# Optimization experiments

Measured on AMD Instinct MI355X. Metric: run time of the kernel, lower is better.

## Reference

```python
import jax, jax.numpy as jnp
import numpy as np

EMBED_DIM = 1024
NUM_HEADS = 16
HEAD_DIM = EMBED_DIM // NUM_HEADS
EPS = 1e-6


def setup_inputs() -> dict:
    key = jax.random.key(0)
    ks = jax.random.split(key, 10)
    B, S, D = 4, 2048, EMBED_DIM
    def xavier(k, shape):
        fan_in, fan_out = shape[1], shape[0]
        limit = float(np.sqrt(6.0 / (fan_in + fan_out)))
        return jax.random.uniform(k, shape, jnp.float32, -limit, limit)
    return {
        "x": jax.random.normal(ks[0], (B, S, D), jnp.float32),
        "ln_gamma": jnp.ones((D,), jnp.float32),
        "ln_beta": jnp.zeros((D,), jnp.float32),
        "Wq": xavier(ks[1], (D, D)), "bq": jnp.zeros((D,), jnp.float32),
        "Wk": xavier(ks[2], (D, D)), "bk": jnp.zeros((D,), jnp.float32),
        "Wv": xavier(ks[3], (D, D)), "bv": jnp.zeros((D,), jnp.float32),
        "Wo": xavier(ks[4], (D, D)), "bo": jnp.zeros((D,), jnp.float32),
    }


def reference(x, ln_gamma, ln_beta, Wq, bq, Wk, bk, Wv, bv, Wo, bo):
    B, S, D = x.shape
    # Pre-LayerNorm
    mu = jnp.mean(x, axis=-1, keepdims=True)
    var = jnp.mean((x - mu) ** 2, axis=-1, keepdims=True)
    xn = (x - mu) / jnp.sqrt(var + EPS) * ln_gamma + ln_beta
    # QKV projections (torch Linear: y = x @ W.T + b)
    def split_heads(t):  # [B,S,D] -> [B,H,S,hd]
        return t.reshape(B, S, NUM_HEADS, HEAD_DIM).transpose(0, 2, 1, 3)
    q = split_heads(xn @ Wq.T + bq)
    k = split_heads(xn @ Wk.T + bk)
    v = split_heads(xn @ Wv.T + bv)
    scale = 1.0 / jnp.sqrt(jnp.float32(HEAD_DIM))
    scores = jnp.einsum("bhqd,bhkd->bhqk", q, k) * scale
    probs = jax.nn.softmax(scores, axis=-1)  # dropout is identity (eval)
    ctx = jnp.einsum("bhqk,bhkd->bhqd", probs, v)
    ctx = ctx.transpose(0, 2, 1, 3).reshape(B, S, D)
    out = ctx @ Wo.T + bo  # proj dropout identity (eval)
    return out
```

## Files before the change

kernel.cpp:

```cpp
#include <hip/hip_runtime.h>
#include <hip/hip_bf16.h>
#include <stdint.h>

typedef __bf16 bf16x8 __attribute__((ext_vector_type(8)));
typedef float f32x4 __attribute__((ext_vector_type(4)));

#define LOG2E 1.44269504088896340736f

__device__ inline void gload_lds16(const void* g, void* l) {
  __builtin_amdgcn_global_load_lds((const __attribute__((address_space(1))) void*)g,
                                   (__attribute__((address_space(3))) void*)l, 16, 0, 0);
}

__device__ inline unsigned short bf16_bits(float f) {
  return __builtin_bit_cast(unsigned short, __float2bfloat16(f));
}

__device__ inline float fast_exp2(float x) {
  return __builtin_amdgcn_exp2f(x);
}

__device__ inline uint32_t cvtpk_bf16(float lo, float hi) {
  uint32_t d;
  asm("v_cvt_pk_bf16_f32 %0, %1, %2" : "=v"(d) : "v"(lo), "v"(hi));
  return d;
}
__device__ inline void plswap32(uint32_t& a, uint32_t& b) {
  asm("v_permlane32_swap_b32 %0, %1" : "+v"(a), "+v"(b));
}
__device__ inline void plswap16(uint32_t& a, uint32_t& b) {
  asm("v_permlane16_swap_b32 %0, %1" : "+v"(a), "+v"(b));
}

__global__ __launch_bounds__(256) void prep_kernel(
    const float* __restrict__ x, const float* __restrict__ gamma,
    const float* __restrict__ beta, __hip_bfloat16* __restrict__ xn,
    const float* __restrict__ Wq, const float* __restrict__ Wk,
    const float* __restrict__ Wv, const float* __restrict__ Wo,
    __hip_bfloat16* __restrict__ Wqk, __hip_bfloat16* __restrict__ Wvb,
    __hip_bfloat16* __restrict__ Wob)
{
  const int t = threadIdx.x;
  if (blockIdx.x < 8192) {
    const int row = blockIdx.x;
    const float4 v = reinterpret_cast<const float4*>(x + (size_t)row * 1024)[t];
    float s = v.x + v.y + v.z + v.w;
    float q = v.x*v.x + v.y*v.y + v.z*v.z + v.w*v.w;
    #pragma unroll
    for (int off = 32; off >= 1; off >>= 1) {
      s += __shfl_xor(s, off);
      q += __shfl_xor(q, off);
    }
    __shared__ float ls[4], lq[4];
    const int wave = t >> 6, lane = t & 63;
    if (lane == 0) { ls[wave] = s; lq[wave] = q; }
    __syncthreads();
    s = ls[0] + ls[1] + ls[2] + ls[3];
    q = lq[0] + lq[1] + lq[2] + lq[3];
    const float mean = s * (1.0f/1024.0f);
    const float var  = q * (1.0f/1024.0f) - mean*mean;
    const float rstd = rsqrtf(var + 1e-6f);
    const float4 gm = reinterpret_cast<const float4*>(gamma)[t];
    const float4 bt = reinterpret_cast<const float4*>(beta)[t];
    ushort4 o;
    o.x = bf16_bits((v.x - mean)*rstd*gm.x + bt.x);
    o.y = bf16_bits((v.y - mean)*rstd*gm.y + bt.y);
    o.z = bf16_bits((v.z - mean)*rstd*gm.z + bt.z);
    o.w = bf16_bits((v.w - mean)*rstd*gm.w + bt.w);
    reinterpret_cast<ushort4*>(xn + (size_t)row*1024)[t] = o;
  } else {
    const int cb = blockIdx.x - 8192;
    const int which = cb >> 10;
    const int i = (cb & 1023) * 256 + t;
    const float* src;
    __hip_bfloat16* dst;
    if (which == 0)      { src = Wq; dst = Wqk; }
    else if (which == 1) { src = Wk; dst = Wqk + 1024*1024; }
    else if (which == 2) { src = Wv; dst = Wvb; }
    else                 { src = Wo; dst = Wob; }
    const float4 v = reinterpret_cast<const float4*>(src)[i];
    ushort4 o;
    o.x = bf16_bits(v.x); o.y = bf16_bits(v.y);
    o.z = bf16_bits(v.z); o.w = bf16_bits(v.w);
    reinterpret_cast<ushort4*>(dst)[i] = o;
  }
}

__global__ __launch_bounds__(256) void qkv_gemm(
    const __hip_bfloat16* __restrict__ xn,
    const __hip_bfloat16* __restrict__ Wqk,
    const __hip_bfloat16* __restrict__ Wvb,
    const float* __restrict__ bq, const float* __restrict__ bk,
    const float* __restrict__ bv,
    __hip_bfloat16* __restrict__ Qb, __hip_bfloat16* __restrict__ Kb,
    __hip_bfloat16* __restrict__ Vt)
{
  constexpr int K = 1024;
  __shared__ __align__(16) __hip_bfloat16 Al[128*32];
  __shared__ __align__(16) __hip_bfloat16 Bl[128*32];
  const int t = threadIdx.x;
  const int wave = t >> 6, lane = t & 63;
  const int li = lane & 15, g = lane >> 4;
  const int wm = (wave >> 1) * 64, wn = (wave & 1) * 64;

  const int lin = blockIdx.x;
  const int wg  = (lin & 7) * 192 + (lin >> 3);
  const bool isV = wg >= 1024;
  int m0, n0;
  const __hip_bfloat16 *A, *B;
  if (!isV) {
    m0 = (wg >> 4) * 128; n0 = (wg & 15) * 128;
    A = xn; B = Wqk;
  } else {
    const int w2 = wg - 1024;
    m0 = (w2 & 7) * 128; n0 = (w2 >> 3) * 128;
    A = Wvb; B = xn;
  }
  const int srow = t >> 2, sch = (t & 3) * 8;

  const __hip_bfloat16* ga = A + (size_t)(m0 + srow) * K + sch;
  const __hip_bfloat16* gb = B + (size_t)(n0 + srow) * K + sch;

  f32x4 acc[4][4] = {};

  for (int kt = 0; kt < K; kt += 32) {
    gload_lds16(ga + kt,          Al + t*8);
    gload_lds16(ga + kt + 64*K,   Al + t*8 + 2048);
    gload_lds16(gb + kt,          Bl + t*8);
    gload_lds16(gb + kt + 64*K,   Bl + t*8 + 2048);
    __syncthreads();
    bf16x8 af[4], bfr[4];
    #pragma unroll
    for (int mi = 0; mi < 4; ++mi)
      af[mi] = *reinterpret_cast<const bf16x8*>(Al + (wm + mi*16 + li)*32 + g*8);
    #pragma unroll
    for (int ni = 0; ni < 4; ++ni)
      bfr[ni] = *reinterpret_cast<const bf16x8*>(Bl + (wn + ni*16 + li)*32 + g*8);
    #pragma unroll
    for (int mi = 0; mi < 4; ++mi)
      #pragma unroll
      for (int ni = 0; ni < 4; ++ni)
        acc[mi][ni] = __builtin_amdgcn_mfma_f32_16x16x32_bf16(af[mi], bfr[ni], acc[mi][ni], 0, 0, 0);
    __syncthreads();
  }

  #pragma unroll
  for (int mi = 0; mi < 4; ++mi) {
    #pragma unroll
    for (int ni = 0; ni < 4; ++ni) {
      #pragma unroll
      for (int r = 0; r < 4; ++r) {
        const int grow = m0 + wm + mi*16 + g*4 + r;
        const int gcol = n0 + wn + ni*16 + li;
        float v = acc[mi][ni][r];
        if (!isV) {
          const int b = grow >> 11, ss = grow & 2047;
          if (gcol < 1024) {
            v = (v + bq[gcol]) * (0.125f * LOG2E);
            const int h = gcol >> 6, d = gcol & 63;
            Qb[(((size_t)(b*16 + h))*2048 + ss)*64 + d] = __float2bfloat16(v);
          } else {
            const int c2 = gcol - 1024;
            v = v + bk[c2];
            const int h = c2 >> 6, d = c2 & 63;
            Kb[(((size_t)(b*16 + h))*2048 + ss)*64 + d] = __float2bfloat16(v);
          }
        } else {
          v += bv[grow];
          Vt[(size_t)grow*8192 + gcol] = __float2bfloat16(v);
        }
      }
    }
  }
}

__global__ __launch_bounds__(256) void out_gemm(
    const __hip_bfloat16* __restrict__ A,
    const __hip_bfloat16* __restrict__ B,
    const float* __restrict__ bias,
    float* __restrict__ C)
{
  constexpr int K = 1024;
  __shared__ __align__(16) __hip_bfloat16 Al[128*32];
  __shared__ __align__(16) __hip_bfloat16 Bl[128*32];
  const int t = threadIdx.x;
  const int wave = t >> 6, lane = t & 63;
  const int li = lane & 15, g = lane >> 4;
  const int wm = (wave >> 1) * 64, wn = (wave & 1) * 64;

  const int lin = blockIdx.y * gridDim.x + blockIdx.x;
  const int cpx = (gridDim.x * gridDim.y) >> 3;
  const int wg  = (lin & 7) * cpx + (lin >> 3);
  const int bx  = wg & (gridDim.x - 1);
  const int by  = wg >> __builtin_ctz(gridDim.x);
  const int m0 = by * 128, n0 = bx * 128;
  const int srow = t >> 2, sch = (t & 3) * 8;

  const __hip_bfloat16* ga = A + (size_t)(m0 + srow) * K + sch;
  const __hip_bfloat16* gb = B + (size_t)(n0 + srow) * K + sch;

  f32x4 acc[4][4] = {};

  for (int kt = 0; kt < K; kt += 32) {
    gload_lds16(ga + kt,          Al + t*8);
    gload_lds16(ga + kt + 64*K,   Al + t*8 + 2048);
    gload_lds16(gb + kt,          Bl + t*8);
    gload_lds16(gb + kt + 64*K,   Bl + t*8 + 2048);
    __syncthreads();
    bf16x8 af[4], bfr[4];
    #pragma unroll
    for (int mi = 0; mi < 4; ++mi)
      af[mi] = *reinterpret_cast<const bf16x8*>(Al + (wm + mi*16 + li)*32 + g*8);
    #pragma unroll
    for (int ni = 0; ni < 4; ++ni)
      bfr[ni] = *reinterpret_cast<const bf16x8*>(Bl + (wn + ni*16 + li)*32 + g*8);
    #pragma unroll
    for (int mi = 0; mi < 4; ++mi)
      #pragma unroll
      for (int ni = 0; ni < 4; ++ni)
        acc[mi][ni] = __builtin_amdgcn_mfma_f32_16x16x32_bf16(af[mi], bfr[ni], acc[mi][ni], 0, 0, 0);
    __syncthreads();
  }

  #pragma unroll
  for (int mi = 0; mi < 4; ++mi) {
    #pragma unroll
    for (int ni = 0; ni < 4; ++ni) {
      #pragma unroll
      for (int r = 0; r < 4; ++r) {
        const int grow = m0 + wm + mi*16 + g*4 + r;
        const int gcol = n0 + wn + ni*16 + li;
        C[(size_t)grow*1024 + gcol] = acc[mi][ni][r] + bias[gcol];
      }
    }
  }
}

__global__ __launch_bounds__(256, 4) void attn_kernel(
    const __hip_bfloat16* __restrict__ Q,
    const __hip_bfloat16* __restrict__ K,
    const __hip_bfloat16* __restrict__ Vt,
    __hip_bfloat16* __restrict__ ctx)
{
  const int t = threadIdx.x, wave = t >> 6, lane = t & 63;
  const int li = lane & 15, g = lane >> 4;

  const int lin = blockIdx.x;
  const int wg  = (lin & 7) * 128 + (lin >> 3);
  const int bh  = wg >> 4, qt = wg & 15;
  const int b = bh >> 4, h = bh & 15;
  const int qbase = qt * 128 + wave * 32;

  __shared__ __align__(16) __hip_bfloat16 Klds[2][4096];
  __shared__ __align__(16) __hip_bfloat16 Vlds[2][4096];

  const bf16x8* Qv0 = reinterpret_cast<const bf16x8*>(Q + ((size_t)bh*2048 + qbase + li)*64 + g*8);
  const bf16x8* Qv1 = reinterpret_cast<const bf16x8*>(Q + ((size_t)bh*2048 + qbase + 16 + li)*64 + g*8);
  const bf16x8 aQ00 = Qv0[0], aQ01 = Qv0[4];
  const bf16x8 aQ10 = Qv1[0], aQ11 = Qv1[4];

  f32x4 acc0[4] = {}, acc1[4] = {};
  float l0 = 0.f, l1 = 0.f;

  const __hip_bfloat16* Kbh = K + (size_t)bh*2048*64;
  const __hip_bfloat16* Vbh = Vt + (size_t)h*64*8192 + b*2048;

  const int l8 = lane >> 3;
  const int scb_e = ((((lane & 7) * 16) ^ (l8 << 4)) >> 1);
  const int row0 = wave * 8 + l8;

  const int krd0 = (li*128 + ((g*16)      ^ ((li & 7) << 4))) >> 1;
  const int krd1 = (li*128 + ((g*16 + 64) ^ ((li & 7) << 4))) >> 1;

  gload_lds16(Kbh + (size_t)row0*64 + scb_e,          &Klds[0][wave*512]);
  gload_lds16(Kbh + (size_t)(32+row0)*64 + scb_e,     &Klds[0][2048 + wave*512]);
  gload_lds16(Vbh + (size_t)row0*8192 + scb_e,        &Vlds[0][wave*512]);
  gload_lds16(Vbh + (size_t)(32+row0)*8192 + scb_e,   &Vlds[0][2048 + wave*512]);
  gload_lds16(Kbh + (size_t)(64+row0)*64 + scb_e,     &Klds[1][wave*512]);
  gload_lds16(Kbh + (size_t)(96+row0)*64 + scb_e,     &Klds[1][2048 + wave*512]);
  gload_lds16(Vbh + (size_t)row0*8192 + 64 + scb_e,   &Vlds[1][wave*512]);
  gload_lds16(Vbh + (size_t)(32+row0)*8192 + 64 + scb_e, &Vlds[1][2048 + wave*512]);
  asm volatile("s_waitcnt vmcnt(4)" ::: "memory");
  __builtin_amdgcn_sched_barrier(0);
  __builtin_amdgcn_s_barrier();

  const __hip_bfloat16* kSrc = Kbh + (size_t)(128 + row0)*64 + scb_e;
  const __hip_bfloat16* vSrc = Vbh + (size_t)row0*8192 + 128 + scb_e;

  for (int it = 0; it < 32; ++it) {
    const int cur = it & 1;
    const __hip_bfloat16* Kc = Klds[cur];
    const __hip_bfloat16* Vc = Vlds[cur];

    f32x4 s0[4] = {}, s1[4] = {};
    __builtin_amdgcn_s_setprio(1);
    #pragma unroll
    for (int nt = 0; nt < 4; ++nt) {
      const bf16x8 k0 = *reinterpret_cast<const bf16x8*>(&Kc[nt*1024 + krd0]);
      const bf16x8 k1 = *reinterpret_cast<const bf16x8*>(&Kc[nt*1024 + krd1]);
      s0[nt] = __builtin_amdgcn_mfma_f32_16x16x32_bf16(k0, aQ00, s0[nt], 0, 0, 0);
      s0[nt] = __builtin_amdgcn_mfma_f32_16x16x32_bf16(k1, aQ01, s0[nt], 0, 0, 0);
      s1[nt] = __builtin_amdgcn_mfma_f32_16x16x32_bf16(k0, aQ10, s1[nt], 0, 0, 0);
      s1[nt] = __builtin_amdgcn_mfma_f32_16x16x32_bf16(k1, aQ11, s1[nt], 0, 0, 0);
    }
    __builtin_amdgcn_s_setprio(0);

    float sm0 = 0.f, sm1 = 0.f;
    #pragma unroll
    for (int nt = 0; nt < 4; ++nt)
      #pragma unroll
      for (int r = 0; r < 4; ++r) {
        const float p0 = fast_exp2(s0[nt][r]); s0[nt][r] = p0; sm0 += p0;
        const float p1 = fast_exp2(s1[nt][r]); s1[nt][r] = p1; sm1 += p1;
      }
    l0 += sm0; l1 += sm1;

    union U8 { uint32_t w[4]; bf16x8 v; };
    bf16x8 aP00, aP01, aP10, aP11;
    {
      uint32_t c[4][2];
      #pragma unroll
      for (int nt = 0; nt < 4; ++nt) {
        c[nt][0] = cvtpk_bf16(s0[nt][0], s0[nt][1]);
        c[nt][1] = cvtpk_bf16(s0[nt][2], s0[nt][3]);
      }
      uint32_t x0 = c[0][0], y0 = c[1][0], x1 = c[0][1], y1 = c[1][1];
      plswap32(x0, y0); plswap32(x1, y1);
      plswap16(x0, y0); plswap16(x1, y1);
      U8 u0; u0.w[0] = x0; u0.w[1] = x1; u0.w[2] = y0; u0.w[3] = y1;
      aP00 = u0.v;
      uint32_t x2 = c[2][0], y2 = c[3][0], x3 = c[2][1], y3 = c[3][1];
      plswap32(x2, y2); plswap32(x3, y3);
      plswap16(x2, y2); plswap16(x3, y3);
      U8 u1; u1.w[0] = x2; u1.w[1] = x3; u1.w[2] = y2; u1.w[3] = y3;
      aP01 = u1.v;
    }
    {
      uint32_t c[4][2];
      #pragma unroll
      for (int nt = 0; nt < 4; ++nt) {
        c[nt][0] = cvtpk_bf16(s1[nt][0], s1[nt][1]);
        c[nt][1] = cvtpk_bf16(s1[nt][2], s1[nt][3]);
      }
      uint32_t x0 = c[0][0], y0 = c[1][0], x1 = c[0][1], y1 = c[1][1];
      plswap32(x0, y0); plswap32(x1, y1);
      plswap16(x0, y0); plswap16(x1, y1);
      U8 u0; u0.w[0] = x0; u0.w[1] = x1; u0.w[2] = y0; u0.w[3] = y1;
      aP10 = u0.v;
      uint32_t x2 = c[2][0], y2 = c[3][0], x3 = c[2][1], y3 = c[3][1];
      plswap32(x2, y2); plswap32(x3, y3);
      plswap16(x2, y2); plswap16(x3, y3);
      U8 u1; u1.w[0] = x2; u1.w[1] = x3; u1.w[2] = y2; u1.w[3] = y3;
      aP11 = u1.v;
    }

    __builtin_amdgcn_s_setprio(1);
    #pragma unroll
    for (int dt = 0; dt < 4; ++dt) {
      const bf16x8 v0 = *reinterpret_cast<const bf16x8*>(&Vc[dt*1024 + krd0]);
      const bf16x8 v1 = *reinterpret_cast<const bf16x8*>(&Vc[dt*1024 + krd1]);
      acc0[dt] = __builtin_amdgcn_mfma_f32_16x16x32_bf16(v0, aP00, acc0[dt], 0, 0, 0);
      acc0[dt] = __builtin_amdgcn_mfma_f32_16x16x32_bf16(v1, aP01, acc0[dt], 0, 0, 0);
      acc1[dt] = __builtin_amdgcn_mfma_f32_16x16x32_bf16(v0, aP10, acc1[dt], 0, 0, 0);
      acc1[dt] = __builtin_amdgcn_mfma_f32_16x16x32_bf16(v1, aP11, acc1[dt], 0, 0, 0);
    }
    __builtin_amdgcn_s_setprio(0);

    if (it < 31) {
      __builtin_amdgcn_s_barrier();
      if (it < 30) {
        gload_lds16(kSrc,           &Klds[cur][wave*512]);
        gload_lds16(kSrc + 32*64,   &Klds[cur][2048 + wave*512]);
        gload_lds16(vSrc,           &Vlds[cur][wave*512]);
        gload_lds16(vSrc + 32*8192, &Vlds[cur][2048 + wave*512]);
        kSrc += 64*64;
        vSrc += 64;
        asm volatile("s_waitcnt vmcnt(4)" ::: "memory");
      } else {
        asm volatile("s_waitcnt vmcnt(0)" ::: "memory");
      }
      __builtin_amdgcn_sched_barrier(0);
      __builtin_amdgcn_s_barrier();
    }
  }

  l0 += __shfl_xor(l0, 16); l0 += __shfl_xor(l0, 32);
  l1 += __shfl_xor(l1, 16); l1 += __shfl_xor(l1, 32);
  const float inv0 = 1.0f / l0;
  const float inv1 = 1.0f / l1;

  __hip_bfloat16* cp = ctx + ((size_t)(b*2048 + qbase))*1024 + h*64;
  #pragma unroll
  for (int dt = 0; dt < 4; ++dt) {
    ushort4 o0, o1;
    o0.x = bf16_bits(acc0[dt][0] * inv0);
    o0.y = bf16_bits(acc0[dt][1] * inv0);
    o0.z = bf16_bits(acc0[dt][2] * inv0);
    o0.w = bf16_bits(acc0[dt][3] * inv0);
    *reinterpret_cast<ushort4*>(&cp[(size_t)li*1024 + dt*16 + g*4]) = o0;
    o1.x = bf16_bits(acc1[dt][0] * inv1);
    o1.y = bf16_bits(acc1[dt][1] * inv1);
    o1.z = bf16_bits(acc1[dt][2] * inv1);
    o1.w = bf16_bits(acc1[dt][3] * inv1);
    *reinterpret_cast<ushort4*>(&cp[(size_t)(16 + li)*1024 + dt*16 + g*4]) = o1;
  }
}

extern "C" void kernel_launch(void* const* d_in, const int* in_sizes, int n_in,
                              void* d_out, int out_size, void* d_ws, size_t ws_size,
                              hipStream_t stream)
{
  const float* x  = (const float*)d_in[0];
  const float* g  = (const float*)d_in[1];
  const float* be = (const float*)d_in[2];
  const float* Wq = (const float*)d_in[3];
  const float* bq = (const float*)d_in[4];
  const float* Wk = (const float*)d_in[5];
  const float* bk = (const float*)d_in[6];
  const float* Wv = (const float*)d_in[7];
  const float* bv = (const float*)d_in[8];
  const float* Wo = (const float*)d_in[9];
  const float* bo = (const float*)d_in[10];
  float* out = (float*)d_out;

  char* ws = (char*)d_ws;
  __hip_bfloat16* xn  = (__hip_bfloat16*)(ws);
  __hip_bfloat16* Wqk = (__hip_bfloat16*)(ws + 16777216);
  __hip_bfloat16* Wvb = (__hip_bfloat16*)(ws + 20971520);
  __hip_bfloat16* Wob = (__hip_bfloat16*)(ws + 23068672);
  __hip_bfloat16* Qb  = (__hip_bfloat16*)(ws + 25165824);
  __hip_bfloat16* Kb  = (__hip_bfloat16*)(ws + 41943040);
  __hip_bfloat16* Vt  = (__hip_bfloat16*)(ws + 58720256);
  __hip_bfloat16* ctx = (__hip_bfloat16*)(ws + 75497472);

  prep_kernel<<<12288, 256, 0, stream>>>(x, g, be, xn, Wq, Wk, Wv, Wo, Wqk, Wvb, Wob);
  qkv_gemm<<<1536, 256, 0, stream>>>(xn, Wqk, Wvb, bq, bk, bv, Qb, Kb, Vt);
  attn_kernel<<<1024, 256, 0, stream>>>(Qb, Kb, Vt, ctx);
  out_gemm<<<dim3(8, 64), 256, 0, stream>>>(ctx, Wob, bo, out);
}
```

Baseline: 198.6 us.

## Split attention query tile across eight waves with 16 rows each

The attention block grows from 4 to 8 waves (512 threads), and each wave now handles 16 query rows instead of 32. K/V tile loads into LDS are spread over all 512 threads, so each thread issues half as many global-to-LDS loads per stage. The aim is more waves in flight and lower per-wave register pressure to hide MFMA and exp latency. The cost is that each K/V LDS fragment now feeds only one 16-row query tile per wave, which halves operand reuse from LDS reads, and the barriers now synchronise twice as many waves.

After: 203.4 us. +2.4%, slower.

```diff
diff --git a/kernel.cpp b/kernel.cpp
--- a/kernel.cpp
+++ b/kernel.cpp
@@ -236,7 +236,7 @@
   }
 }
 
-__global__ __launch_bounds__(256, 4) void attn_kernel(
+__global__ __launch_bounds__(512, 8) void attn_kernel(
     const __hip_bfloat16* __restrict__ Q,
     const __hip_bfloat16* __restrict__ K,
     const __hip_bfloat16* __restrict__ Vt,
@@ -249,38 +249,31 @@
   const int wg  = (lin & 7) * 128 + (lin >> 3);
   const int bh  = wg >> 4, qt = wg & 15;
   const int b = bh >> 4, h = bh & 15;
-  const int qbase = qt * 128 + wave * 32;
+  const int qbase = qt * 128 + wave * 16;
 
   __shared__ __align__(16) __hip_bfloat16 Klds[2][4096];
   __shared__ __align__(16) __hip_bfloat16 Vlds[2][4096];
 
-  const bf16x8* Qv0 = reinterpret_cast<const bf16x8*>(Q + ((size_t)bh*2048 + qbase + li)*64 + g*8);
-  const bf16x8* Qv1 = reinterpret_cast<const bf16x8*>(Q + ((size_t)bh*2048 + qbase + 16 + li)*64 + g*8);
-  const bf16x8 aQ00 = Qv0[0], aQ01 = Qv0[4];
-  const bf16x8 aQ10 = Qv1[0], aQ11 = Qv1[4];
-
-  f32x4 acc0[4] = {}, acc1[4] = {};
-  float l0 = 0.f, l1 = 0.f;
+  const bf16x8* Qv = reinterpret_cast<const bf16x8*>(Q + ((size_t)bh*2048 + qbase + li)*64 + g*8);
+  const bf16x8 aQ0 = Qv[0], aQ1 = Qv[4];
+
+  f32x4 acc[4] = {};
+  float l_par = 0.f;
 
   const __hip_bfloat16* Kbh = K + (size_t)bh*2048*64;
   const __hip_bfloat16* Vbh = Vt + (size_t)h*64*8192 + b*2048;
 
-  const int l8 = lane >> 3;
-  const int scb_e = ((((lane & 7) * 16) ^ (l8 << 4)) >> 1);
-  const int row0 = wave * 8 + l8;
+  const int row0 = t >> 3;
+  const int scb_e = ((((t & 7) * 16) ^ ((row0 & 7) << 4)) >> 1);
 
   const int krd0 = (li*128 + ((g*16)      ^ ((li & 7) << 4))) >> 1;
   const int krd1 = (li*128 + ((g*16 + 64) ^ ((li & 7) << 4))) >> 1;
 
-  gload_lds16(Kbh + (size_t)row0*64 + scb_e,          &Klds[0][wave*512]);
-  gload_lds16(Kbh + (size_t)(32+row0)*64 + scb_e,     &Klds[0][2048 + wave*512]);
-  gload_lds16(Vbh + (size_t)row0*8192 + scb_e,        &Vlds[0][wave*512]);
-  gload_lds16(Vbh + (size_t)(32+row0)*8192 + scb_e,   &Vlds[0][2048 + wave*512]);
-  gload_lds16(Kbh + (size_t)(64+row0)*64 + scb_e,     &Klds[1][wave*512]);
-  gload_lds16(Kbh + (size_t)(96+row0)*64 + scb_e,     &Klds[1][2048 + wave*512]);
-  gload_lds16(Vbh + (size_t)row0*8192 + 64 + scb_e,   &Vlds[1][wave*512]);
-  gload_lds16(Vbh + (size_t)(32+row0)*8192 + 64 + scb_e, &Vlds[1][2048 + wave*512]);
-  asm volatile("s_waitcnt vmcnt(4)" ::: "memory");
+  gload_lds16(Kbh + (size_t)row0*64 + scb_e,        &Klds[0][t*8]);
+  gload_lds16(Vbh + (size_t)row0*8192 + scb_e,      &Vlds[0][t*8]);
+  gload_lds16(Kbh + (size_t)(64+row0)*64 + scb_e,   &Klds[1][t*8]);
+  gload_lds16(Vbh + (size_t)row0*8192 + 64 + scb_e, &Vlds[1][t*8]);
+  asm volatile("s_waitcnt vmcnt(2)" ::: "memory");
   __builtin_amdgcn_sched_barrier(0);
   __builtin_amdgcn_s_barrier();
 
@@ -292,66 +285,45 @@
     const __hip_bfloat16* Kc = Klds[cur];
     const __hip_bfloat16* Vc = Vlds[cur];
 
-    f32x4 s0[4] = {}, s1[4] = {};
+    f32x4 s[4] = {};
     __builtin_amdgcn_s_setprio(1);
     #pragma unroll
     for (int nt = 0; nt < 4; ++nt) {
       const bf16x8 k0 = *reinterpret_cast<const bf16x8*>(&Kc[nt*1024 + krd0]);
       const bf16x8 k1 = *reinterpret_cast<const bf16x8*>(&Kc[nt*1024 + krd1]);
-      s0[nt] = __builtin_amdgcn_mfma_f32_16x16x32_bf16(k0, aQ00, s0[nt], 0, 0, 0);
-      s0[nt] = __builtin_amdgcn_mfma_f32_16x16x32_bf16(k1, aQ01, s0[nt], 0, 0, 0);
-      s1[nt] = __builtin_amdgcn_mfma_f32_16x16x32_bf16(k0, aQ10, s1[nt], 0, 0, 0);
-      s1[nt] = __builtin_amdgcn_mfma_f32_16x16x32_bf16(k1, aQ11, s1[nt], 0, 0, 0);
+      s[nt] = __builtin_amdgcn_mfma_f32_16x16x32_bf16(k0, aQ0, s[nt], 0, 0, 0);
+      s[nt] = __builtin_amdgcn_mfma_f32_16x16x32_bf16(k1, aQ1, s[nt], 0, 0, 0);
     }
     __builtin_amdgcn_s_setprio(0);
 
-    float sm0 = 0.f, sm1 = 0.f;
+    float sm = 0.f;
     #pragma unroll
     for (int nt = 0; nt < 4; ++nt)
       #pragma unroll
       for (int r = 0; r < 4; ++r) {
-        const float p0 = fast_exp2(s0[nt][r]); s0[nt][r] = p0; sm0 += p0;
-        const float p1 = fast_exp2(s1[nt][r]); s1[nt][r] = p1; sm1 += p1;
+        const float p = fast_exp2(s[nt][r]); s[nt][r] = p; sm += p;
       }
-    l0 += sm0; l1 += sm1;
+    l_par += sm;
 
     union U8 { uint32_t w[4]; bf16x8 v; };
-    bf16x8 aP00, aP01, aP10, aP11;
+    bf16x8 aP0, aP1;
     {
       uint32_t c[4][2];
       #pragma unroll
       for (int nt = 0; nt < 4; ++nt) {
-        c[nt][0] = cvtpk_bf16(s0[nt][0], s0[nt][1]);
-        c[nt][1] = cvtpk_bf16(s0[nt][2], s0[nt][3]);
+        c[nt][0] = cvtpk_bf16(s[nt][0], s[nt][1]);
+        c[nt][1] = cvtpk_bf16(s[nt][2], s[nt][3]);
       }
       uint32_t x0 = c[0][0], y0 = c[1][0], x1 = c[0][1], y1 = c[1][1];
       plswap32(x0, y0); plswap32(x1, y1);
       plswap16(x0, y0); plswap16(x1, y1);
       U8 u0; u0.w[0] = x0; u0.w[1] = x1; u0.w[2] = y0; u0.w[3] = y1;
-      aP00 = u0.v;
+      aP0 = u0.v;
       uint32_t x2 = c[2][0], y2 = c[3][0], x3 = c[2][1], y3 = c[3][1];
       plswap32(x2, y2); plswap32(x3, y3);
       plswap16(x2, y2); plswap16(x3, y3);
       U8 u1; u1.w[0] = x2; u1.w[1] = x3; u1.w[2] = y2; u1.w[3] = y3;
-      aP01 = u1.v;
-    }
-    {
-      uint32_t c[4][2];
-      #pragma unroll
-      for (int nt = 0; nt < 4; ++nt) {
-        c[nt][0] = cvtpk_bf16(s1[nt][0], s1[nt][1]);
-        c[nt][1] = cvtpk_bf16(s1[nt][2], s1[nt][3]);
-      }
-      uint32_t x0 = c[0][0], y0 = c[1][0], x1 = c[0][1], y1 = c[1][1];
-      plswap32(x0, y0); plswap32(x1, y1);
-      plswap16(x0, y0); plswap16(x1, y1);
-      U8 u0; u0.w[0] = x0; u0.w[1] = x1; u0.w[2] = y0; u0.w[3] = y1;
-      aP10 = u0.v;
-      uint32_t x2 = c[2][0], y2 = c[3][0], x3 = c[2][1], y3 = c[3][1];
-      plswap32(x2, y2); plswap32(x3, y3);
-      plswap16(x2, y2); plswap16(x3, y3);
-      U8 u1; u1.w[0] = x2; u1.w[1] = x3; u1.w[2] = y2; u1.w[3] = y3;
-      aP11 = u1.v;
+      aP1 = u1.v;
     }
 
     __builtin_amdgcn_s_setprio(1);
@@ -359,23 +331,19 @@
     for (int dt = 0; dt < 4; ++dt) {
       const bf16x8 v0 = *reinterpret_cast<const bf16x8*>(&Vc[dt*1024 + krd0]);
       const bf16x8 v1 = *reinterpret_cast<const bf16x8*>(&Vc[dt*1024 + krd1]);
-      acc0[dt] = __builtin_amdgcn_mfma_f32_16x16x32_bf16(v0, aP00, acc0[dt], 0, 0, 0);
-      acc0[dt] = __builtin_amdgcn_mfma_f32_16x16x32_bf16(v1, aP01, acc0[dt], 0, 0, 0);
-      acc1[dt] = __builtin_amdgcn_mfma_f32_16x16x32_bf16(v0, aP10, acc1[dt], 0, 0, 0);
-      acc1[dt] = __builtin_amdgcn_mfma_f32_16x16x32_bf16(v1, aP11, acc1[dt], 0, 0, 0);
+      acc[dt] = __builtin_amdgcn_mfma_f32_16x16x32_bf16(v0, aP0, acc[dt], 0, 0, 0);
+      acc[dt] = __builtin_amdgcn_mfma_f32_16x16x32_bf16(v1, aP1, acc[dt], 0, 0, 0);
     }
     __builtin_amdgcn_s_setprio(0);
 
     if (it < 31) {
       __builtin_amdgcn_s_barrier();
       if (it < 30) {
-        gload_lds16(kSrc,           &Klds[cur][wave*512]);
-        gload_lds16(kSrc + 32*64,   &Klds[cur][2048 + wave*512]);
-        gload_lds16(vSrc,           &Vlds[cur][wave*512]);
-        gload_lds16(vSrc + 32*8192, &Vlds[cur][2048 + wave*512]);
+        gload_lds16(kSrc, &Klds[cur][t*8]);
+        gload_lds16(vSrc, &Vlds[cur][t*8]);
         kSrc += 64*64;
         vSrc += 64;
-        asm volatile("s_waitcnt vmcnt(4)" ::: "memory");
+        asm volatile("s_waitcnt vmcnt(2)" ::: "memory");
       } else {
         asm volatile("s_waitcnt vmcnt(0)" ::: "memory");
       }
@@ -384,25 +352,19 @@
     }
   }
 
-  l0 += __shfl_xor(l0, 16); l0 += __shfl_xor(l0, 32);
-  l1 += __shfl_xor(l1, 16); l1 += __shfl_xor(l1, 32);
-  const float inv0 = 1.0f / l0;
-  const float inv1 = 1.0f / l1;
+  l_par += __shfl_xor(l_par, 16);
+  l_par += __shfl_xor(l_par, 32);
+  const float inv = 1.0f / l_par;
 
   __hip_bfloat16* cp = ctx + ((size_t)(b*2048 + qbase))*1024 + h*64;
   #pragma unroll
   for (int dt = 0; dt < 4; ++dt) {
-    ushort4 o0, o1;
-    o0.x = bf16_bits(acc0[dt][0] * inv0);
-    o0.y = bf16_bits(acc0[dt][1] * inv0);
-    o0.z = bf16_bits(acc0[dt][2] * inv0);
-    o0.w = bf16_bits(acc0[dt][3] * inv0);
-    *reinterpret_cast<ushort4*>(&cp[(size_t)li*1024 + dt*16 + g*4]) = o0;
-    o1.x = bf16_bits(acc1[dt][0] * inv1);
-    o1.y = bf16_bits(acc1[dt][1] * inv1);
-    o1.z = bf16_bits(acc1[dt][2] * inv1);
-    o1.w = bf16_bits(acc1[dt][3] * inv1);
-    *reinterpret_cast<ushort4*>(&cp[(size_t)(16 + li)*1024 + dt*16 + g*4]) = o1;
+    ushort4 o;
+    o.x = bf16_bits(acc[dt][0] * inv);
+    o.y = bf16_bits(acc[dt][1] * inv);
+    o.z = bf16_bits(acc[dt][2] * inv);
+    o.w = bf16_bits(acc[dt][3] * inv);
+    *reinterpret_cast<ushort4*>(&cp[(size_t)li*1024 + dt*16 + g*4]) = o;
   }
 }
 
@@ -435,6 +397,6 @@
 
   prep_kernel<<<12288, 256, 0, stream>>>(x, g, be, xn, Wq, Wk, Wv, Wo, Wqk, Wvb, Wob);
   qkv_gemm<<<1536, 256, 0, stream>>>(xn, Wqk, Wvb, bq, bk, bv, Qb, Kb, Vt);
-  attn_kernel<<<1024, 256, 0, stream>>>(Qb, Kb, Vt, ctx);
+  attn_kernel<<<1024, 512, 0, stream>>>(Qb, Kb, Vt, ctx);
   out_gemm<<<dim3(8, 64), 256, 0, stream>>>(ctx, Wob, bo, out);
 }
```
